# Optimization experiments

Measured on AMD Instinct MI355X. Metric: run time of the kernel, lower is better.

## Reference

```python
import jax, jax.numpy as jnp
import numpy as np

B, T, E, H, W = 2, 1024, 1024, 8, 31
D = 2 * W + 1  # head dim must equal 2*window_size+1 for the rel-pos broadcast


def _ln(x, w, b):
    mu = jnp.mean(x, axis=-1, keepdims=True)
    var = jnp.mean(jnp.square(x - mu), axis=-1, keepdims=True)
    return (x - mu) * jax.lax.rsqrt(var + 1e-5) * w + b


def setup_inputs() -> dict:
    key = jax.random.key(0)
    k = jax.random.split(key, 8)
    s = 0.02
    return {
        "x": jax.random.normal(k[0], (B, T, E // 2), jnp.float32),
        "ln1_w": jnp.ones(E, jnp.float32), "ln1_b": jnp.zeros(E, jnp.float32),
        "qkv_w": jax.random.normal(k[1], (3 * H * D, E), jnp.float32) * s,
        "qkv_b": jnp.zeros(3 * H * D, jnp.float32),
        "rel_pos": jax.random.normal(k[2], (D, D), jnp.float32) * s,
        "proj_w": jax.random.normal(k[3], (E, H * D), jnp.float32) * s,
        "proj_b": jnp.zeros(E, jnp.float32),
        "ln2_w": jnp.ones(E, jnp.float32), "ln2_b": jnp.zeros(E, jnp.float32),
        "fc_w": jax.random.normal(k[4], (4 * E, E), jnp.float32) * s,
        "fc_b": jnp.zeros(4 * E, jnp.float32),
        "cproj_w": jax.random.normal(k[5], (E, 4 * E), jnp.float32) * s,
        "cproj_b": jnp.zeros(E, jnp.float32),
    }


def reference(x, ln1_w, ln1_b, qkv_w, qkv_b, rel_pos, proj_w, proj_b,
              ln2_w, ln2_b, fc_w, fc_b, cproj_w, cproj_b):
    # --- RotaryEmbedding: angle = x * inv_freq; out = cat(sin, cos) -> [B,T,E]
    dim = 2 * x.shape[-1]
    inv_freq = 1.0 / 10000.0 ** (jnp.arange(0, dim, 2, dtype=jnp.float32) / dim)
    ang = x * inv_freq
    xr = jnp.concatenate([jnp.sin(ang), jnp.cos(ang)], axis=-1)  # [B,T,E]

    # --- custom windowed attention on ln_1(xr)
    h = _ln(xr, ln1_w, ln1_b)
    qkv = h @ qkv_w.T + qkv_b                       # [B,T,3*H*D]
    q, k, v = jnp.split(qkv, 3, axis=-1)

    def heads(t):
        return t.reshape(B, T, H, D).transpose(0, 2, 1, 3)  # [B,H,T,D]

    q, k, v = heads(q), heads(k), heads(v)
    # per-token q-outer-k scores (einsum '...bd,...bv->...bdv'): [B,H,T,D,D]
    scores = jnp.einsum('bhtd,bhtv->bhtdv', q, k)
    # rel-pos bias: Embedding lookup at offsets -W..W (negative indices wrap)
    bias = rel_pos[jnp.arange(-W, W + 1) % D]       # [D, D] == [2W+1, d_model]
    attn = jax.nn.softmax(scores + bias, axis=-2)   # softmax over non-canonical axis
    out = jnp.einsum('bhtdv,bhtv->bhtd', attn, v)   # apply per-token attn matrix to v
    out = out.transpose(0, 2, 1, 3).reshape(B, T, H * D)
    xa = xr + out @ proj_w.T + proj_b               # residual

    # --- MLP
    h2 = _ln(xa, ln2_w, ln2_b)
    m = jax.nn.gelu(h2 @ fc_w.T + fc_b, approximate=False) @ cproj_w.T + cproj_b
    return xa + m
```

## Files before the change

kernel.cpp:

```cpp
#include <hip/hip_runtime.h>
#include <hip/hip_bf16.h>


typedef __bf16 bf16;
typedef bf16 bf16x8 __attribute__((ext_vector_type(8)));
typedef bf16 bf16x4 __attribute__((ext_vector_type(4)));
typedef bf16 bf16x2 __attribute__((ext_vector_type(2)));
typedef float f32x4 __attribute__((ext_vector_type(4)));

__device__ __forceinline__ float rdlane(float x, int l)
{
    return __int_as_float(__builtin_amdgcn_readlane(__float_as_int(x), l));
}

__global__ __launch_bounds__(256) void rotary_ln_kernel(
    const float* __restrict__ x, const float* __restrict__ w,
    const float* __restrict__ b, float* __restrict__ xr, bf16* __restrict__ Y)
{
    const int row = blockIdx.x;
    const int tid = threadIdx.x;
    float2 xv = *(const float2*)(x + (size_t)row * 512 + tid * 2);
    float i0 = exp2f(-(float)(2*tid)     * 0.025952563241307518f);
    float i1 = exp2f(-(float)(2*tid + 1) * 0.025952563241307518f);
    float a0 = xv.x * i0, a1 = xv.y * i1;
    float s0 = sinf(a0), s1 = sinf(a1);
    float c0 = cosf(a0), c1 = cosf(a1);
    *(float2*)(xr + (size_t)row * 1024 + tid*2)       = make_float2(s0, s1);
    *(float2*)(xr + (size_t)row * 1024 + 512 + tid*2) = make_float2(c0, c1);
    float s  = s0 + s1 + c0 + c1;
    float ss = s0*s0 + s1*s1 + c0*c0 + c1*c1;
    #pragma unroll
    for (int off = 32; off > 0; off >>= 1) {
        s  += __shfl_down(s, off);
        ss += __shfl_down(ss, off);
    }
    __shared__ float rs[4], rss[4];
    int wave = tid >> 6, lane = tid & 63;
    if (lane == 0) { rs[wave] = s; rss[wave] = ss; }
    __syncthreads();
    s  = rs[0] + rs[1] + rs[2] + rs[3];
    ss = rss[0] + rss[1] + rss[2] + rss[3];
    float mu   = s * (1.f / 1024.f);
    float var  = ss * (1.f / 1024.f) - mu * mu;
    float rstd = rsqrtf(var + 1e-5f);
    float2 w0 = *(const float2*)(w + tid*2);
    float2 b0 = *(const float2*)(b + tid*2);
    float2 w1 = *(const float2*)(w + 512 + tid*2);
    float2 b1 = *(const float2*)(b + 512 + tid*2);
    bf16x2 y0, y1;
    y0[0] = (bf16)((s0 - mu) * rstd * w0.x + b0.x);
    y0[1] = (bf16)((s1 - mu) * rstd * w0.y + b0.y);
    y1[0] = (bf16)((c0 - mu) * rstd * w1.x + b1.x);
    y1[1] = (bf16)((c1 - mu) * rstd * w1.y + b1.y);
    *(bf16x2*)(Y + (size_t)row * 1024 + tid*2)       = y0;
    *(bf16x2*)(Y + (size_t)row * 1024 + 512 + tid*2) = y1;
}

__device__ __forceinline__ void conv_chunk(
    const float* __restrict__ src, bf16* __restrict__ dst,
    int ci, int N, int K, int Kp)
{
    int kpc = Kp >> 3;
    int r  = ci / kpc;
    int kc = (ci - r * kpc) << 3;
    bf16x8 o;
    if (r < N && kc < K) {
        float4 f0 = *(const float4*)(src + (size_t)r * K + kc);
        float4 f1 = *(const float4*)(src + (size_t)r * K + kc + 4);
        o[0]=(bf16)f0.x; o[1]=(bf16)f0.y; o[2]=(bf16)f0.z; o[3]=(bf16)f0.w;
        o[4]=(bf16)f1.x; o[5]=(bf16)f1.y; o[6]=(bf16)f1.z; o[7]=(bf16)f1.w;
    } else {
        #pragma unroll
        for (int j = 0; j < 8; ++j) o[j] = (bf16)0.f;
    }
    *(bf16x8*)(dst + (size_t)r * Kp + kc) = o;
}

__global__ __launch_bounds__(256) void conv_all_kernel(
    const float* __restrict__ qkv_w, const float* __restrict__ proj_w,
    const float* __restrict__ fc_w,  const float* __restrict__ cproj_w,
    const float* __restrict__ qkv_b,
    bf16* __restrict__ wqkv, bf16* __restrict__ wproj,
    bf16* __restrict__ wfc,  bf16* __restrict__ wcproj,
    float* __restrict__ qkvb_p)
{
    if (blockIdx.x == 5120) {
        for (int i = threadIdx.x; i < 1536; i += 256)
            qkvb_p[i] = (i < 1512) ? qkv_b[i] : 0.f;
        return;
    }
    int idx = blockIdx.x * 256 + threadIdx.x;
    if      (idx < 196608)  conv_chunk(qkv_w,   wqkv,   idx,          1512, 1024, 1024);
    else if (idx < 262144)  conv_chunk(proj_w,  wproj,  idx - 196608, 1024,  504,  512);
    else if (idx < 786432)  conv_chunk(fc_w,    wfc,    idx - 262144, 4096, 1024, 1024);
    else                    conv_chunk(cproj_w, wcproj, idx - 786432, 1024, 4096, 4096);
}

template<int N> __device__ __forceinline__ void vmwait()
{
    if constexpr      (N==0) asm volatile("s_waitcnt vmcnt(0)" ::: "memory");
    else if constexpr (N==3) asm volatile("s_waitcnt vmcnt(3)" ::: "memory");
}
__device__ __forceinline__ void lgkmwait0()
{
    asm volatile("s_waitcnt lgkmcnt(0)" ::: "memory");
}
__device__ __forceinline__ void hw_barrier()
{
    asm volatile("s_barrier" ::: "memory");
}
__device__ __forceinline__ void gload16(const char* src, char* ldsdst)
{
    __builtin_amdgcn_global_load_lds(
        (const __attribute__((address_space(1))) void*)src,
        (__attribute__((address_space(3))) void*)ldsdst, 16, 0, 0);
}
__device__ __forceinline__ float gelu_exact(float v)
{
    return 0.5f * v * (1.f + erff(v * 0.70710678118654752f));
}

template<int EPI>
__global__ __launch_bounds__(256, 4) void gemm7_kernel(
    const bf16* __restrict__ A, const bf16* __restrict__ Wt,
    const float* __restrict__ bias, bf16* __restrict__ Cb,
    int N, int Kp, int ksplit)
{
    __shared__ __align__(16) char lds[3][12288];

    const int tid  = threadIdx.x;
    const int w    = tid >> 6;
    const int lane = tid & 63;

    const int gx = gridDim.x, gy = gridDim.y;
    const int nwg = gx * gy * gridDim.z;
    const int chunk = nwg >> 3;
    int id = (blockIdx.z * gy + blockIdx.y) * gx + blockIdx.x;
    int sw = (id & 7) * chunk + (id >> 3);
    const int bx = sw % gx;
    const int t2 = sw / gx;
    const int by = t2 % gy;
    const int bz = t2 / gy;

    const int row0 = by * 64;
    const int col0 = bx * 128;
    const int wr = (w >> 1) * 32;
    const int wc = (w & 1) * 64;
    const int rl = lane & 15;
    const int slotR = lane >> 4;

    const size_t strideBy = (size_t)Kp * 2;
    const size_t kz = (size_t)bz * ksplit * 2;
    const char* Abase = (const char*)A  + (size_t)row0 * strideBy + kz;
    const char* Wbase = (const char*)Wt + (size_t)col0 * strideBy + kz;

    const int arow = tid >> 2;
    const size_t srcA0 = (size_t)arow * strideBy
                       + (size_t)(((tid & 3) ^ ((arow >> 1) & 3)) << 4);
    size_t srcB[2];
    #pragma unroll
    for (int i = 0; i < 2; ++i) {
        int o = (i * 256 + tid) * 16;
        int r = o >> 6;
        int s = ((o & 63) >> 4) ^ ((r >> 1) & 3);
        srcB[i] = (size_t)r * strideBy + (size_t)(s << 4);
    }

    f32x4 acc[2][4] = {};

    auto STAGE = [&](int buf, int kt) {
        const char* ab = Abase + (size_t)kt * 64;
        const char* wb = Wbase + (size_t)kt * 64;
        gload16(ab + srcA0, &lds[buf][0] + tid * 16);
        #pragma unroll
        for (int i = 0; i < 2; ++i)
            gload16(wb + srcB[i], &lds[buf][4096] + (i * 256 + tid) * 16);
    };

    const int niter = ksplit >> 5;
    STAGE(0, 0);
    STAGE(1, 1);
    vmwait<3>();
    hw_barrier();

    int cur = 0, stg = 2;
    for (int kt = 0; kt < niter; ++kt) {
        if (kt + 2 < niter) STAGE(stg, kt + 2);
        const char* base = lds[cur];
        bf16x8 af[2], bfr[4];
        #pragma unroll
        for (int mi = 0; mi < 2; ++mi) {
            int r = wr + mi * 16 + rl;
            af[mi] = *(const bf16x8*)
                (base + (r << 6) + ((slotR ^ ((r >> 1) & 3)) << 4));
        }
        #pragma unroll
        for (int nj = 0; nj < 4; ++nj) {
            int r = wc + nj * 16 + rl;
            bfr[nj] = *(const bf16x8*)
                (base + 4096 + (r << 6) + ((slotR ^ ((r >> 1) & 3)) << 4));
        }
        __builtin_amdgcn_s_setprio(1);
        #pragma unroll
        for (int mi = 0; mi < 2; ++mi)
            #pragma unroll
            for (int nj = 0; nj < 4; ++nj)
                acc[mi][nj] = __builtin_amdgcn_mfma_f32_16x16x32_bf16(
                    af[mi], bfr[nj], acc[mi][nj], 0, 0, 0);
        __builtin_amdgcn_s_setprio(0);

        if (kt + 1 < niter) {
            lgkmwait0();
            if (kt + 2 < niter) vmwait<3>();
            else                vmwait<0>();
            hw_barrier();
        }
        cur = (cur == 2) ? 0 : cur + 1;
        stg = (stg == 2) ? 0 : stg + 1;
    }

    const int rq = (lane >> 4) * 4;
    bf16* Cbz = Cb;
    if (EPI == 3) Cbz += (size_t)bz * 2048 * N;
    #pragma unroll
    for (int mi = 0; mi < 2; ++mi) {
        #pragma unroll
        for (int rj = 0; rj < 4; ++rj) {
            int row = row0 + wr + mi*16 + rq + rj;
            #pragma unroll
            for (int nj = 0; nj < 4; ++nj) {
                int col = col0 + wc + nj*16 + rl;
                float c = acc[mi][nj][rj];
                size_t off = (size_t)row * N + col;
                if (EPI == 0)      Cbz[off] = (bf16)(c + bias[col]);
                else if (EPI == 1) Cbz[off] = (bf16)gelu_exact(c + bias[col]);
                else               Cbz[off] = (bf16)c;
            }
        }
    }
}

template<int P>
__global__ __launch_bounds__(256) void reduce_kernel(
    const bf16* __restrict__ parts, const float* __restrict__ bias,
    const float* R, float* out)
{
    int row = blockIdx.x;
    int c = threadIdx.x * 4;
    size_t off = (size_t)row * 1024 + c;
    float4 bv = *(const float4*)(bias + c);
    float4 o = *(const float4*)(R + off);
    o.x += bv.x; o.y += bv.y; o.z += bv.z; o.w += bv.w;
    #pragma unroll
    for (int p = 0; p < P; ++p) {
        bf16x4 v = *(const bf16x4*)(parts + (size_t)p * 2048 * 1024 + off);
        o.x += (float)v[0]; o.y += (float)v[1];
        o.z += (float)v[2]; o.w += (float)v[3];
    }
    *(float4*)(out + off) = o;
}

__global__ __launch_bounds__(256) void reduceln_kernel(
    const bf16* __restrict__ parts, const float* __restrict__ bias,
    const float* __restrict__ R, const float* __restrict__ lnw,
    const float* __restrict__ lnb, float* __restrict__ out,
    bf16* __restrict__ Y)
{
    int row = blockIdx.x;
    int c = threadIdx.x * 4;
    size_t off = (size_t)row * 1024 + c;
    float4 bv = *(const float4*)(bias + c);
    float4 o  = *(const float4*)(R + off);
    o.x += bv.x; o.y += bv.y; o.z += bv.z; o.w += bv.w;
    #pragma unroll
    for (int p = 0; p < 2; ++p) {
        bf16x4 v = *(const bf16x4*)(parts + (size_t)p * 2048 * 1024 + off);
        o.x += (float)v[0]; o.y += (float)v[1];
        o.z += (float)v[2]; o.w += (float)v[3];
    }
    *(float4*)(out + off) = o;
    float s  = o.x + o.y + o.z + o.w;
    float ss = o.x*o.x + o.y*o.y + o.z*o.z + o.w*o.w;
    #pragma unroll
    for (int of = 32; of > 0; of >>= 1) {
        s  += __shfl_down(s, of);
        ss += __shfl_down(ss, of);
    }
    __shared__ float rs[4], rss[4];
    int wave = threadIdx.x >> 6, lane = threadIdx.x & 63;
    if (lane == 0) { rs[wave] = s; rss[wave] = ss; }
    __syncthreads();
    s  = rs[0] + rs[1] + rs[2] + rs[3];
    ss = rss[0] + rss[1] + rss[2] + rss[3];
    float mu  = s * (1.f / 1024.f);
    float var = ss * (1.f / 1024.f) - mu * mu;
    float rstd = rsqrtf(var + 1e-5f);
    float4 wv = *(const float4*)(lnw + c);
    float4 lb = *(const float4*)(lnb + c);
    bf16 y[4];
    y[0] = (bf16)((o.x - mu) * rstd * wv.x + lb.x);
    y[1] = (bf16)((o.y - mu) * rstd * wv.y + lb.y);
    y[2] = (bf16)((o.z - mu) * rstd * wv.z + lb.z);
    y[3] = (bf16)((o.w - mu) * rstd * wv.w + lb.w);
    *(uint2*)(Y + (size_t)row * 1024 + c) = *(uint2*)y;
}

__global__ __launch_bounds__(1024) void attn3_kernel(
    const bf16* __restrict__ qkv, const float* __restrict__ rel_pos,
    bf16* __restrict__ outp)
{
    __shared__ float bR[4096];
    __shared__ float bT[4096];
    for (int i = threadIdx.x; i < 4096; i += 1024) {
        int d = i >> 6, v = i & 63;
        float val = (d < 63 && v < 63)
                  ? rel_pos[((d + 32) % 63) * 63 + v] * 1.4426950408889634f
                  : -1e30f;
        bR[(d << 6) + (((v >> 2) ^ (d & 15)) << 2) + (v & 3)] = val;
        bT[(v << 6) + (((d >> 2) ^ (v & 15)) << 2) + (d & 3)] = val;
    }
    __syncthreads();

    const int wave = threadIdx.x >> 6;
    const int lane = threadIdx.x & 63;
    const int tk  = blockIdx.x * 16 + wave;
    const int row = tk >> 3;
    const int h   = tk & 7;
    const bf16* base = qkv + (size_t)row * 1536 + h * 63;
    float q_own = 0.f, k_own = 0.f, v_own = 0.f;
    if (lane < 63) {
        q_own = (float)base[lane] * 1.4426950408889634f;
        k_own = (float)base[504 + lane];
        v_own = (float)base[1008 + lane];
    }

    const float* myT = bT + (lane << 6);
    const int sw = lane & 15;
    float z0 = 0.f, z1 = 0.f, z2 = 0.f, z3 = 0.f;
    #pragma unroll
    for (int g = 0; g < 16; ++g) {
        f32x4 bb = *(const f32x4*)(myT + ((g ^ sw) << 2));
        z0 += __builtin_amdgcn_exp2f(fmaf(rdlane(q_own, 4*g + 0), k_own, bb[0]));
        z1 += __builtin_amdgcn_exp2f(fmaf(rdlane(q_own, 4*g + 1), k_own, bb[1]));
        z2 += __builtin_amdgcn_exp2f(fmaf(rdlane(q_own, 4*g + 2), k_own, bb[2]));
        z3 += __builtin_amdgcn_exp2f(fmaf(rdlane(q_own, 4*g + 3), k_own, bb[3]));
    }
    float Z = (z0 + z1) + (z2 + z3);
    float w_own = (lane < 63) ? v_own / Z : 0.f;

    const float* myR = bR + (lane << 6);
    float a0 = 0.f, a1 = 0.f, a2 = 0.f, a3 = 0.f;
    #pragma unroll
    for (int g = 0; g < 16; ++g) {
        f32x4 bb = *(const f32x4*)(myR + ((g ^ sw) << 2));
        a0 = fmaf(__builtin_amdgcn_exp2f(fmaf(q_own, rdlane(k_own, 4*g + 0), bb[0])),
                  rdlane(w_own, 4*g + 0), a0);
        a1 = fmaf(__builtin_amdgcn_exp2f(fmaf(q_own, rdlane(k_own, 4*g + 1), bb[1])),
                  rdlane(w_own, 4*g + 1), a1);
        a2 = fmaf(__builtin_amdgcn_exp2f(fmaf(q_own, rdlane(k_own, 4*g + 2), bb[2])),
                  rdlane(w_own, 4*g + 2), a2);
        a3 = fmaf(__builtin_amdgcn_exp2f(fmaf(q_own, rdlane(k_own, 4*g + 3), bb[3])),
                  rdlane(w_own, 4*g + 3), a3);
    }
    float acc = (a0 + a1) + (a2 + a3);

    if (lane < 63)
        outp[(size_t)row * 512 + h*63 + lane] = (bf16)acc;
    if (h == 7 && lane == 63) {
        #pragma unroll
        for (int j = 0; j < 8; ++j)
            outp[(size_t)row * 512 + 504 + j] = (bf16)0.f;
    }
}

extern "C" void kernel_launch(void* const* d_in, const int* in_sizes, int n_in,
                              void* d_out, int out_size, void* d_ws, size_t ws_size,
                              hipStream_t stream)
{
    const float* x       = (const float*)d_in[0];
    const float* ln1_w   = (const float*)d_in[1];
    const float* ln1_b   = (const float*)d_in[2];
    const float* qkv_w   = (const float*)d_in[3];
    const float* qkv_b   = (const float*)d_in[4];
    const float* rel_pos = (const float*)d_in[5];
    const float* proj_w  = (const float*)d_in[6];
    const float* proj_b  = (const float*)d_in[7];
    const float* ln2_w   = (const float*)d_in[8];
    const float* ln2_b   = (const float*)d_in[9];
    const float* fc_w    = (const float*)d_in[10];
    const float* fc_b    = (const float*)d_in[11];
    const float* cproj_w = (const float*)d_in[12];
    const float* cproj_b = (const float*)d_in[13];
    float* out = (float*)d_out;

    char* p = (char*)d_ws;
    float* xr      = (float*)p;            p += (size_t)2048*1024*4;
    bf16*  h_bf    = (bf16*)p;             p += (size_t)2048*1024*2;
    bf16*  wqkv    = (bf16*)p;             p += (size_t)1536*1024*2;
    bf16*  wproj   = (bf16*)p;             p += (size_t)1024*512*2;
    bf16*  wfc     = (bf16*)p;             p += (size_t)4096*1024*2;
    bf16*  wcproj  = (bf16*)p;             p += (size_t)1024*4096*2;
    float* qkvb_p  = (float*)p;            p += 8192;
    bf16*  attn_bf = (bf16*)p;             p += (size_t)2048*512*2;
    bf16*  qkvb    = (bf16*)p;
    bf16*  fc_act  = (bf16*)p;
    bf16*  proj_part = qkvb;
    bf16*  cp_part = (bf16*)d_ws;

    conv_all_kernel<<<5121, 256, 0, stream>>>(qkv_w, proj_w, fc_w, cproj_w, qkv_b,
                                              wqkv, wproj, wfc, wcproj, qkvb_p);
    rotary_ln_kernel<<<2048, 256, 0, stream>>>(x, ln1_w, ln1_b, xr, h_bf);
    gemm7_kernel<0><<<dim3(12,32,1), 256, 0, stream>>>(h_bf, wqkv, qkvb_p,
                                                       qkvb, 1536, 1024, 1024);
    attn3_kernel<<<1024, 1024, 0, stream>>>(qkvb, rel_pos, attn_bf);
    gemm7_kernel<3><<<dim3(8,32,2), 256, 0, stream>>>(attn_bf, wproj, nullptr,
                                                      proj_part, 1024, 512, 256);
    reduceln_kernel<<<2048, 256, 0, stream>>>(proj_part, proj_b, xr,
                                              ln2_w, ln2_b, out, h_bf);
    gemm7_kernel<1><<<dim3(32,32,1), 256, 0, stream>>>(h_bf, wfc, fc_b,
                                                       fc_act, 4096, 1024, 1024);
    gemm7_kernel<3><<<dim3(8,32,4), 256, 0, stream>>>(fc_act, wcproj, nullptr,
                                                      cp_part, 1024, 4096, 1024);
    reduce_kernel<4><<<2048, 256, 0, stream>>>(cp_part, cproj_b, out, out);
}
```

Before: 149.4 us.

## Use 128x128 tiled GEMM kernel for MLP fc and cproj layers

Adds a new GEMM kernel with 128x128 output tiles per workgroup (each wave computes a 64x64 sub-tile with 4x4 MFMAs), triple-buffered LDS staging via direct global-to-LDS loads, and XOR-swizzled reads. The MLP fc and cproj GEMMs switch to it with halved row-block grids. The aim is to raise operand reuse per loaded byte and cut global/LDS traffic. In exchange it uses more registers and LDS, lowering occupancy to 3 workgroups per CU and leaving fewer workgroups to fill the GPU.

```diff
diff --git a/kernel.cpp b/kernel.cpp
--- a/kernel.cpp
+++ b/kernel.cpp
@@ -100,6 +100,7 @@
 {
     if constexpr      (N==0) asm volatile("s_waitcnt vmcnt(0)" ::: "memory");
     else if constexpr (N==3) asm volatile("s_waitcnt vmcnt(3)" ::: "memory");
+    else if constexpr (N==4) asm volatile("s_waitcnt vmcnt(4)" ::: "memory");
 }
 __device__ __forceinline__ void lgkmwait0()
 {
@@ -118,6 +119,126 @@
 __device__ __forceinline__ float gelu_exact(float v)
 {
     return 0.5f * v * (1.f + erff(v * 0.70710678118654752f));
+}
+
+template<int EPI>
+__global__ __launch_bounds__(256, 3) void gemm9_kernel(
+    const bf16* __restrict__ A, const bf16* __restrict__ Wt,
+    const float* __restrict__ bias, bf16* __restrict__ Cb,
+    int N, int Kp, int ksplit)
+{
+    __shared__ __align__(16) char lds[3][16384];
+
+    const int tid  = threadIdx.x;
+    const int w    = tid >> 6;
+    const int lane = tid & 63;
+
+    const int gx = gridDim.x, gy = gridDim.y;
+    const int nwg = gx * gy * gridDim.z;
+    const int chunk = nwg >> 3;
+    int id = (blockIdx.z * gy + blockIdx.y) * gx + blockIdx.x;
+    int sw = (id & 7) * chunk + (id >> 3);
+    const int bx = sw % gx;
+    const int t2 = sw / gx;
+    const int by = t2 % gy;
+    const int bz = t2 / gy;
+
+    const int row0 = by * 128;
+    const int col0 = bx * 128;
+    const int wr = (w >> 1) * 64;
+    const int wc = (w & 1) * 64;
+    const int rl = lane & 15;
+    const int slotR = lane >> 4;
+
+    const size_t strideBy = (size_t)Kp * 2;
+    const size_t kz = (size_t)bz * ksplit * 2;
+    const char* Abase = (const char*)A  + (size_t)row0 * strideBy + kz;
+    const char* Wbase = (const char*)Wt + (size_t)col0 * strideBy + kz;
+
+    size_t srcA[2];
+    #pragma unroll
+    for (int i = 0; i < 2; ++i) {
+        int ch = i * 256 + tid;
+        int r  = ch >> 2;
+        int s  = (ch & 3) ^ ((r >> 1) & 3);
+        srcA[i] = (size_t)r * strideBy + (size_t)(s << 4);
+    }
+
+    f32x4 acc[4][4] = {};
+
+    auto STAGE = [&](int buf, int kt) {
+        const char* ab = Abase + (size_t)kt * 64;
+        const char* wb = Wbase + (size_t)kt * 64;
+        #pragma unroll
+        for (int i = 0; i < 2; ++i)
+            gload16(ab + srcA[i], &lds[buf][0]    + (i * 256 + tid) * 16);
+        #pragma unroll
+        for (int i = 0; i < 2; ++i)
+            gload16(wb + srcA[i], &lds[buf][8192] + (i * 256 + tid) * 16);
+    };
+
+    const int niter = ksplit >> 5;
+    STAGE(0, 0);
+    STAGE(1, 1);
+    vmwait<4>();
+    hw_barrier();
+
+    int cur = 0, stg = 2;
+    for (int kt = 0; kt < niter; ++kt) {
+        if (kt + 2 < niter) STAGE(stg, kt + 2);
+        const char* base = lds[cur];
+        bf16x8 af[4], bfr[4];
+        #pragma unroll
+        for (int mi = 0; mi < 4; ++mi) {
+            int r = wr + mi * 16 + rl;
+            af[mi] = *(const bf16x8*)
+                (base + (r << 6) + ((slotR ^ ((r >> 1) & 3)) << 4));
+        }
+        #pragma unroll
+        for (int nj = 0; nj < 4; ++nj) {
+            int r = wc + nj * 16 + rl;
+            bfr[nj] = *(const bf16x8*)
+                (base + 8192 + (r << 6) + ((slotR ^ ((r >> 1) & 3)) << 4));
+        }
+        hw_barrier();
+        lgkmwait0();
+        __builtin_amdgcn_s_setprio(1);
+        #pragma unroll
+        for (int mi = 0; mi < 4; ++mi)
+            #pragma unroll
+            for (int nj = 0; nj < 4; ++nj)
+                acc[mi][nj] = __builtin_amdgcn_mfma_f32_16x16x32_bf16(
+                    af[mi], bfr[nj], acc[mi][nj], 0, 0, 0);
+        __builtin_amdgcn_s_setprio(0);
+
+        if (kt + 1 < niter) {
+            if (kt + 2 < niter) vmwait<4>();
+            else                vmwait<0>();
+            hw_barrier();
+        }
+        cur = (cur == 2) ? 0 : cur + 1;
+        stg = (stg == 2) ? 0 : stg + 1;
+    }
+
+    const int rq = (lane >> 4) * 4;
+    bf16* Cbz = Cb;
+    if (EPI == 3) Cbz += (size_t)bz * 2048 * N;
+    #pragma unroll
+    for (int mi = 0; mi < 4; ++mi) {
+        #pragma unroll
+        for (int rj = 0; rj < 4; ++rj) {
+            int row = row0 + wr + mi*16 + rq + rj;
+            #pragma unroll
+            for (int nj = 0; nj < 4; ++nj) {
+                int col = col0 + wc + nj*16 + rl;
+                float c = acc[mi][nj][rj];
+                size_t off = (size_t)row * N + col;
+                if (EPI == 0)      Cbz[off] = (bf16)(c + bias[col]);
+                else if (EPI == 1) Cbz[off] = (bf16)gelu_exact(c + bias[col]);
+                else               Cbz[off] = (bf16)c;
+            }
+        }
+    }
 }
 
 template<int EPI>
@@ -417,9 +538,9 @@
                                                       proj_part, 1024, 512, 256);
     reduceln_kernel<<<2048, 256, 0, stream>>>(proj_part, proj_b, xr,
                                               ln2_w, ln2_b, out, h_bf);
-    gemm7_kernel<1><<<dim3(32,32,1), 256, 0, stream>>>(h_bf, wfc, fc_b,
+    gemm9_kernel<1><<<dim3(32,16,1), 256, 0, stream>>>(h_bf, wfc, fc_b,
                                                        fc_act, 4096, 1024, 1024);
-    gemm7_kernel<3><<<dim3(8,32,4), 256, 0, stream>>>(fc_act, wcproj, nullptr,
+    gemm9_kernel<3><<<dim3(8,16,4), 256, 0, stream>>>(fc_act, wcproj, nullptr,
                                                       cp_part, 1024, 4096, 1024);
     reduce_kernel<4><<<2048, 256, 0, stream>>>(cp_part, cproj_b, out, out);
 }
```

New measurement: 136.9 us. -8.4%, faster.
